# Kernel optimization log

Hardware: AMD Instinct MI355X
Metric: run time of the kernel (lower is better)

## Reference

```python
import jax, jax.numpy as jnp
import numpy as np

HEADS = 16
ROT_DIM = 32  # RotaryEmbedding(dim=32), interleaved (GPT-J style) as in rotary_embedding_torch
THETA = 10000.0


def _rope(x):
    # x: (B, H, S, hd); rotate first ROT_DIM dims, pass through the rest
    S = x.shape[-2]
    inv_freq = 1.0 / (THETA ** (jnp.arange(0, ROT_DIM, 2, dtype=jnp.float32) / ROT_DIM))  # (ROT_DIM/2,)
    ang = jnp.arange(S, dtype=jnp.float32)[:, None] * inv_freq[None, :]                   # (S, ROT_DIM/2)
    ang = jnp.repeat(ang, 2, axis=-1)                                                     # (S, ROT_DIM) interleaved
    cos, sin = jnp.cos(ang), jnp.sin(ang)
    xr, xp = x[..., :ROT_DIM], x[..., ROT_DIM:]
    # rotate_half, interleaved pairs: (x1, x2) -> (-x2, x1)
    x2 = xr.reshape(*xr.shape[:-1], ROT_DIM // 2, 2)
    xr_half = jnp.stack([-x2[..., 1], x2[..., 0]], axis=-1).reshape(xr.shape)
    xr = xr * cos + xr_half * sin
    return jnp.concatenate([xr, xp], axis=-1)


def _split_heads(x, H):
    # (S, B, D) -> (B, H, S, hd)
    S, B, D = x.shape
    return x.transpose(1, 0, 2).reshape(B, S, H, D // H).transpose(0, 2, 1, 3)


def setup_inputs() -> dict:
    key = jax.random.key(0)
    ks = jax.random.split(key, 11)
    S, B, D = 2048, 2, 1024
    f = lambda k, shp, s=1.0: jax.random.normal(k, shp, dtype=jnp.float32) * s
    return {
        "Q": f(ks[0], (S, B, D)),
        "K": f(ks[1], (S, B, D)),
        "V": f(ks[2], (S, B, D)),
        "Wq": f(ks[3], (D, D), 0.02), "bq": f(ks[4], (D,), 0.02),
        "Wk": f(ks[5], (D, D), 0.02), "bk": f(ks[6], (D,), 0.02),
        "Wv": f(ks[7], (D, D), 0.02), "bv": f(ks[8], (D,), 0.02),
        "Wo": f(ks[9], (D, D), 0.02), "bo": f(ks[10], (D,), 0.02),
    }


def reference(Q, K, V, Wq, bq, Wk, bk, Wv, bv, Wo, bo):
    S, B, D = Q.shape
    H = HEADS
    hd = D // H
    q = _rope(_split_heads(Q @ Wq.T + bq, H))   # (B, H, S, hd)
    k = _rope(_split_heads(K @ Wk.T + bk, H))
    v = _split_heads(V @ Wv.T + bv, H)
    scores = jnp.einsum("bhqd,bhkd->bhqk", q, k) / jnp.sqrt(jnp.float32(hd))
    probs = jax.nn.softmax(scores, axis=-1)
    out = jnp.einsum("bhqk,bhkd->bhqd", probs, v)  # (B, H, S, hd)
    out = out.transpose(0, 2, 1, 3).reshape(B, S, D).transpose(1, 0, 2)  # (S, B, D)
    return out @ Wo.T + bo
```

## Files before the change

### kernel.cpp

```cpp
#include <hip/hip_runtime.h>
#include <hip/hip_bf16.h>
#include <hip/hip_fp16.h>

#define S_LEN  2048
#define BATCH  2
#define DMODEL 1024
#define NHEADS 16
#define HD     64
#define MROWS  4096
#define LD     72
#define NT     (S_LEN / 64)

using f16 = _Float16;
typedef __attribute__((ext_vector_type(8))) _Float16 f16x8;
typedef __attribute__((ext_vector_type(4))) _Float16 f16x4;
typedef __attribute__((ext_vector_type(4))) float    f32x4;

__device__ __forceinline__ void gload16(const void* g, void* l)
{
    __builtin_amdgcn_global_load_lds((const __attribute__((address_space(1))) void*)g,
                                     (__attribute__((address_space(3))) void*)l, 16, 0, 0);
}

__global__ __launch_bounds__(256) void rope_table(float* __restrict__ rc, float* __restrict__ rs)
{
    int idx = blockIdx.x * 256 + threadIdx.x;
    int s = idx >> 4, i = idx & 15;
    float inv = powf(10000.0f, -(float)(2 * i) / 32.0f);
    float ang = (float)s * inv;
    rc[idx] = cosf(ang);
    rs[idx] = sinf(ang);
}

__global__ __launch_bounds__(256) void cvt_all(
    const float* __restrict__ Q, const float* __restrict__ K, const float* __restrict__ V,
    const float* __restrict__ Wq, const float* __restrict__ Wk, const float* __restrict__ Wv,
    const float* __restrict__ Wo, f16* __restrict__ dst)
{
    const int z = blockIdx.y;
    const float* src; size_t off; int n8;
    switch (z) {
        case 0:  src = Q;  off = 0;        n8 = 524288; break;
        case 1:  src = K;  off = 4194304;  n8 = 524288; break;
        case 2:  src = V;  off = 8388608;  n8 = 524288; break;
        case 3:  src = Wq; off = 12582912; n8 = 131072; break;
        case 4:  src = Wk; off = 13631488; n8 = 131072; break;
        case 5:  src = Wv; off = 14680064; n8 = 131072; break;
        default: src = Wo; off = 15728640; n8 = 131072; break;
    }
    int i = blockIdx.x * 256 + threadIdx.x;
    if (i >= n8) return;
    const float4* s = reinterpret_cast<const float4*>(src) + (size_t)i * 2;
    float4 v0 = s[0], v1 = s[1];
    f16x8 h = { (f16)v0.x, (f16)v0.y, (f16)v0.z, (f16)v0.w,
                (f16)v1.x, (f16)v1.y, (f16)v1.z, (f16)v1.w };
    reinterpret_cast<f16x8*>(dst + off)[i] = h;
}

__global__ __launch_bounds__(256) void proj_gemm_h(
    const f16* __restrict__ Xq, const f16* __restrict__ Xk, const f16* __restrict__ Xv,
    const f16* __restrict__ Wq, const f16* __restrict__ Wk, const f16* __restrict__ Wv,
    const float* __restrict__ bq, const float* __restrict__ bk, const float* __restrict__ bv,
    f16* __restrict__ qo, f16* __restrict__ ko, f16* __restrict__ vo,
    const float* __restrict__ rc, const float* __restrict__ rs)
{
    const int mode = blockIdx.z;
    const f16* X     = (mode == 0) ? Xq : (mode == 1) ? Xk : Xv;
    const f16* W     = (mode == 0) ? Wq : (mode == 1) ? Wk : Wv;
    const float* bias = (mode == 0) ? bq : (mode == 1) ? bk : bv;

    __shared__ f16 Al[128 * 32];
    __shared__ f16 Bl[128 * 32];

    const int t = threadIdx.x, lane = t & 63, wid = t >> 6;
    const int q15 = lane & 15, g = lane >> 4;
    const int wr = wid >> 1, wc = wid & 1;
    const int m0 = blockIdx.x * 128, n0 = blockIdx.y * 128;

    const int srow = wid * 16 + (lane >> 2);
    const int scol = (lane & 3) * 8;
    const f16* Xg = X + (size_t)(m0 + srow) * DMODEL + scol;
    const f16* Wg = W + (size_t)(n0 + srow) * DMODEL + scol;
    f16* al0 = &Al[(wid * 16) * 32];
    f16* al1 = &Al[(wid * 16 + 64) * 32];
    f16* bl0 = &Bl[(wid * 16) * 32];
    f16* bl1 = &Bl[(wid * 16 + 64) * 32];

    f32x4 acc[4][4];
    #pragma unroll
    for (int m = 0; m < 4; m++)
        #pragma unroll
        for (int n = 0; n < 4; n++)
            acc[m][n] = f32x4{0.f, 0.f, 0.f, 0.f};

    for (int k0 = 0; k0 < DMODEL; k0 += 32) {
        __syncthreads();
        gload16(Xg + k0, al0);
        gload16(Xg + (size_t)64 * DMODEL + k0, al1);
        gload16(Wg + k0, bl0);
        gload16(Wg + (size_t)64 * DMODEL + k0, bl1);
        __syncthreads();

        f16x8 a[4], b[4];
        #pragma unroll
        for (int m = 0; m < 4; m++)
            a[m] = *reinterpret_cast<const f16x8*>(&Al[(wr * 64 + m * 16 + q15) * 32 + g * 8]);
        #pragma unroll
        for (int n = 0; n < 4; n++)
            b[n] = *reinterpret_cast<const f16x8*>(&Bl[(wc * 64 + n * 16 + q15) * 32 + g * 8]);
        #pragma unroll
        for (int m = 0; m < 4; m++)
            #pragma unroll
            for (int n = 0; n < 4; n++)
                acc[m][n] = __builtin_amdgcn_mfma_f32_16x16x32_f16(a[m], b[n], acc[m][n], 0, 0, 0);
    }

    const int rowb = m0 + wr * 64, colb = n0 + wc * 64;
    #pragma unroll
    for (int n = 0; n < 4; n++) {
        int cN = colb + n * 16 + q15;
        float bvv = bias[cN];
        int h = cN >> 6, d = cN & 63;
        #pragma unroll
        for (int m = 0; m < 4; m++) {
            #pragma unroll
            for (int rg = 0; rg < 4; rg++) {
                int r = rowb + m * 16 + g * 4 + rg;
                int s = r >> 1, bi = r & 1;
                float val = acc[m][n][rg] + bvv;
                if (mode < 2) {
                    float pv = __shfl_xor(val, 1);
                    if (d < 32) {
                        int fi = d >> 1;
                        float cc = rc[s * 16 + fi], ss = rs[s * 16 + fi];
                        val = ((d & 1) == 0) ? val * cc - pv * ss : val * cc + pv * ss;
                    }
                    if (mode == 0) val *= 0.18033688f;
                    ((mode == 0) ? qo : ko)[(((size_t)bi * NHEADS + h) * S_LEN + s) * HD + d] = (f16)val;
                } else {
                    vo[(((size_t)bi * NHEADS + h) * HD + d) * S_LEN + s] = (f16)val;
                }
            }
        }
    }
}

__global__ __launch_bounds__(256) void out_gemm_h(
    const f16* __restrict__ X, const f16* __restrict__ W,
    const float* __restrict__ bias, float* __restrict__ out)
{
    __shared__ f16 Al[128 * 32];
    __shared__ f16 Bl[128 * 32];

    const int t = threadIdx.x, lane = t & 63, wid = t >> 6;
    const int q15 = lane & 15, g = lane >> 4;
    const int wr = wid >> 1, wc = wid & 1;
    const int m0 = blockIdx.x * 128, n0 = blockIdx.y * 128;

    const int srow = wid * 16 + (lane >> 2);
    const int scol = (lane & 3) * 8;
    const f16* Xg = X + (size_t)(m0 + srow) * DMODEL + scol;
    const f16* Wg = W + (size_t)(n0 + srow) * DMODEL + scol;
    f16* al0 = &Al[(wid * 16) * 32];
    f16* al1 = &Al[(wid * 16 + 64) * 32];
    f16* bl0 = &Bl[(wid * 16) * 32];
    f16* bl1 = &Bl[(wid * 16 + 64) * 32];

    f32x4 acc[4][4];
    #pragma unroll
    for (int m = 0; m < 4; m++)
        #pragma unroll
        for (int n = 0; n < 4; n++)
            acc[m][n] = f32x4{0.f, 0.f, 0.f, 0.f};

    for (int k0 = 0; k0 < DMODEL; k0 += 32) {
        __syncthreads();
        gload16(Xg + k0, al0);
        gload16(Xg + (size_t)64 * DMODEL + k0, al1);
        gload16(Wg + k0, bl0);
        gload16(Wg + (size_t)64 * DMODEL + k0, bl1);
        __syncthreads();

        f16x8 a[4], b[4];
        #pragma unroll
        for (int m = 0; m < 4; m++)
            a[m] = *reinterpret_cast<const f16x8*>(&Al[(wr * 64 + m * 16 + q15) * 32 + g * 8]);
        #pragma unroll
        for (int n = 0; n < 4; n++)
            b[n] = *reinterpret_cast<const f16x8*>(&Bl[(wc * 64 + n * 16 + q15) * 32 + g * 8]);
        #pragma unroll
        for (int m = 0; m < 4; m++)
            #pragma unroll
            for (int n = 0; n < 4; n++)
                acc[m][n] = __builtin_amdgcn_mfma_f32_16x16x32_f16(a[m], b[n], acc[m][n], 0, 0, 0);
    }

    const int rowb = m0 + wr * 64, colb = n0 + wc * 64;
    #pragma unroll
    for (int n = 0; n < 4; n++) {
        int cN = colb + n * 16 + q15;
        float bvv = bias[cN];
        #pragma unroll
        for (int m = 0; m < 4; m++) {
            #pragma unroll
            for (int rg = 0; rg < 4; rg++) {
                int r = rowb + m * 16 + g * 4 + rg;
                out[(size_t)r * DMODEL + cN] = acc[m][n][rg] + bvv;
            }
        }
    }
}

__global__ __launch_bounds__(256) void proj_gemm(
    const float* __restrict__ Xq, const float* __restrict__ Xk, const float* __restrict__ Xv,
    const float* __restrict__ Wq, const float* __restrict__ Wk, const float* __restrict__ Wv,
    const float* __restrict__ bq, const float* __restrict__ bk, const float* __restrict__ bv,
    f16* __restrict__ qo, f16* __restrict__ ko, f16* __restrict__ vo,
    const float* __restrict__ rc, const float* __restrict__ rs)
{
    const int mode = blockIdx.z;
    const float* X    = (mode == 0) ? Xq : (mode == 1) ? Xk : Xv;
    const float* W    = (mode == 0) ? Wq : (mode == 1) ? Wk : Wv;
    const float* bias = (mode == 0) ? bq : (mode == 1) ? bk : bv;

    __shared__ f16 Al[128 * 40];
    __shared__ f16 Bl[128 * 40];

    const int t = threadIdx.x;
    const int lane = t & 63, wid = t >> 6;
    const int wr = wid >> 1, wc = wid & 1;
    const int m0 = blockIdx.x * 128, n0 = blockIdx.y * 128;

    f32x4 acc[4][4];
    #pragma unroll
    for (int m = 0; m < 4; m++)
        #pragma unroll
        for (int n = 0; n < 4; n++)
            acc[m][n] = f32x4{0.f, 0.f, 0.f, 0.f};

    for (int k0 = 0; k0 < DMODEL; k0 += 32) {
        __syncthreads();
        #pragma unroll
        for (int i = 0; i < 2; i++) {
            int e = (i * 256 + t) * 8;
            int r = e >> 5, c = e & 31;
            {
                const float* src = &X[(size_t)(m0 + r) * DMODEL + k0 + c];
                float4 v0 = *reinterpret_cast<const float4*>(src);
                float4 v1 = *reinterpret_cast<const float4*>(src + 4);
                f16x8 h = { (f16)v0.x, (f16)v0.y, (f16)v0.z, (f16)v0.w,
                            (f16)v1.x, (f16)v1.y, (f16)v1.z, (f16)v1.w };
                *reinterpret_cast<f16x8*>(&Al[r * 40 + c]) = h;
            }
            {
                const float* src = &W[(size_t)(n0 + r) * DMODEL + k0 + c];
                float4 v0 = *reinterpret_cast<const float4*>(src);
                float4 v1 = *reinterpret_cast<const float4*>(src + 4);
                f16x8 h = { (f16)v0.x, (f16)v0.y, (f16)v0.z, (f16)v0.w,
                            (f16)v1.x, (f16)v1.y, (f16)v1.z, (f16)v1.w };
                *reinterpret_cast<f16x8*>(&Bl[r * 40 + c]) = h;
            }
        }
        __syncthreads();
        f16x8 a[4], b[4];
        #pragma unroll
        for (int m = 0; m < 4; m++)
            a[m] = *reinterpret_cast<const f16x8*>(&Al[(wr * 64 + m * 16 + (lane & 15)) * 40 + (lane >> 4) * 8]);
        #pragma unroll
        for (int n = 0; n < 4; n++)
            b[n] = *reinterpret_cast<const f16x8*>(&Bl[(wc * 64 + n * 16 + (lane & 15)) * 40 + (lane >> 4) * 8]);
        #pragma unroll
        for (int m = 0; m < 4; m++)
            #pragma unroll
            for (int n = 0; n < 4; n++)
                acc[m][n] = __builtin_amdgcn_mfma_f32_16x16x32_f16(a[m], b[n], acc[m][n], 0, 0, 0);
    }

    const int rowb = m0 + wr * 64, colb = n0 + wc * 64;
    #pragma unroll
    for (int n = 0; n < 4; n++) {
        int cN = colb + n * 16 + (lane & 15);
        float bvv = bias[cN];
        int h = cN >> 6, d = cN & 63;
        #pragma unroll
        for (int m = 0; m < 4; m++) {
            #pragma unroll
            for (int rg = 0; rg < 4; rg++) {
                int r = rowb + m * 16 + (lane >> 4) * 4 + rg;
                int s = r >> 1, bi = r & 1;
                float val = acc[m][n][rg] + bvv;
                if (mode < 2) {
                    float pv = __shfl_xor(val, 1);
                    if (d < 32) {
                        int fi = d >> 1;
                        float cc = rc[s * 16 + fi], ss = rs[s * 16 + fi];
                        val = ((d & 1) == 0) ? val * cc - pv * ss : val * cc + pv * ss;
                    }
                    if (mode == 0) val *= 0.18033688f;
                    ((mode == 0) ? qo : ko)[(((size_t)bi * NHEADS + h) * S_LEN + s) * HD + d] = (f16)val;
                } else {
                    vo[(((size_t)bi * NHEADS + h) * HD + d) * S_LEN + s] = (f16)val;
                }
            }
        }
    }
}

__global__ __launch_bounds__(256) void out_gemm(
    const f16* __restrict__ X, const float* __restrict__ W,
    const float* __restrict__ bias, float* __restrict__ out)
{
    __shared__ f16 Al[128 * 40];
    __shared__ f16 Bl[128 * 40];

    const int t = threadIdx.x;
    const int lane = t & 63, wid = t >> 6;
    const int wr = wid >> 1, wc = wid & 1;
    const int m0 = blockIdx.x * 128, n0 = blockIdx.y * 128;

    f32x4 acc[4][4];
    #pragma unroll
    for (int m = 0; m < 4; m++)
        #pragma unroll
        for (int n = 0; n < 4; n++)
            acc[m][n] = f32x4{0.f, 0.f, 0.f, 0.f};

    for (int k0 = 0; k0 < DMODEL; k0 += 32) {
        __syncthreads();
        #pragma unroll
        for (int i = 0; i < 2; i++) {
            int e = (i * 256 + t) * 8;
            int r = e >> 5, c = e & 31;
            *reinterpret_cast<uint4*>(&Al[r * 40 + c]) =
                *reinterpret_cast<const uint4*>(&X[(size_t)(m0 + r) * DMODEL + k0 + c]);
            {
                const float* src = &W[(size_t)(n0 + r) * DMODEL + k0 + c];
                float4 v0 = *reinterpret_cast<const float4*>(src);
                float4 v1 = *reinterpret_cast<const float4*>(src + 4);
                f16x8 h = { (f16)v0.x, (f16)v0.y, (f16)v0.z, (f16)v0.w,
                            (f16)v1.x, (f16)v1.y, (f16)v1.z, (f16)v1.w };
                *reinterpret_cast<f16x8*>(&Bl[r * 40 + c]) = h;
            }
        }
        __syncthreads();
        f16x8 a[4], b[4];
        #pragma unroll
        for (int m = 0; m < 4; m++)
            a[m] = *reinterpret_cast<const f16x8*>(&Al[(wr * 64 + m * 16 + (lane & 15)) * 40 + (lane >> 4) * 8]);
        #pragma unroll
        for (int n = 0; n < 4; n++)
            b[n] = *reinterpret_cast<const f16x8*>(&Bl[(wc * 64 + n * 16 + (lane & 15)) * 40 + (lane >> 4) * 8]);
        #pragma unroll
        for (int m = 0; m < 4; m++)
            #pragma unroll
            for (int n = 0; n < 4; n++)
                acc[m][n] = __builtin_amdgcn_mfma_f32_16x16x32_f16(a[m], b[n], acc[m][n], 0, 0, 0);
    }

    const int rowb = m0 + wr * 64, colb = n0 + wc * 64;
    #pragma unroll
    for (int n = 0; n < 4; n++) {
        int cN = colb + n * 16 + (lane & 15);
        float bvv = bias[cN];
        #pragma unroll
        for (int m = 0; m < 4; m++) {
            #pragma unroll
            for (int rg = 0; rg < 4; rg++) {
                int r = rowb + m * 16 + (lane >> 4) * 4 + rg;
                out[(size_t)r * DMODEL + cN] = acc[m][n][rg] + bvv;
            }
        }
    }
}

__global__ __launch_bounds__(512) void attn_fwd(
    const f16* __restrict__ qb, const f16* __restrict__ kb,
    const f16* __restrict__ vt, f16* __restrict__ ctx)
{
    __shared__ f16 Kl[2][64 * 64];
    __shared__ f16 Vl[3][64 * 64];
    __shared__ f16 Pl[2][8 * 16 * LD];

    const int t = threadIdx.x, lane = t & 63, wid = t >> 6;
    const int q15 = lane & 15, g = lane >> 4;
    const int sw = q15 & 7;
    const int bh = blockIdx.y;
    const int q0 = blockIdx.x * 128 + wid * 16;

    const f16* qptr = qb + ((size_t)bh * S_LEN + q0) * HD;
    f16x8 qf0 = *reinterpret_cast<const f16x8*>(&qptr[q15 * HD + g * 8]);
    f16x8 qf1 = *reinterpret_cast<const f16x8*>(&qptr[q15 * HD + g * 8 + 32]);

    f32x4 ctxa[4];
    #pragma unroll
    for (int i = 0; i < 4; i++) ctxa[i] = f32x4{0.f, 0.f, 0.f, 0.f};
    float mrun = -3.0e38f, lrun = 0.f;

    const int srow = t >> 3;
    const int sslot = (t & 7) ^ (srow & 7);
    const f16* kg = kb + (size_t)bh * S_LEN * HD + (size_t)srow * HD + sslot * 8;
    const f16* vg = vt + (size_t)bh * HD * S_LEN + (size_t)srow * S_LEN + sslot * 8;
    const int lds_wbase = wid * 512;
    const int poff = wid * (16 * LD);

    gload16(kg, &Kl[0][lds_wbase]);
    gload16(vg, &Vl[0][lds_wbase]);
    __syncthreads();

    int kbuf = 0;
    int vprev = 2, vcur = 0, vnext = 1;

    for (int kt = 0; kt < NT; kt++) {
        if (kt + 1 < NT) {
            gload16(kg + (size_t)(kt + 1) * 64 * HD, &Kl[kbuf ^ 1][lds_wbase]);
            gload16(vg + (size_t)(kt + 1) * 64,      &Vl[vnext][lds_wbase]);
        }
        const f16* Kc = Kl[kbuf];

        f32x4 sc[4];
        __builtin_amdgcn_s_setprio(1);
        #pragma unroll
        for (int f = 0; f < 4; f++) {
            f16x8 kf0 = *reinterpret_cast<const f16x8*>(&Kc[(f * 16 + q15) * 64 + ((g ^ sw) * 8)]);
            f16x8 kf1 = *reinterpret_cast<const f16x8*>(&Kc[(f * 16 + q15) * 64 + (((g + 4) ^ sw) * 8)]);
            f32x4 z = {0.f, 0.f, 0.f, 0.f};
            z = __builtin_amdgcn_mfma_f32_16x16x32_f16(kf0, qf0, z, 0, 0, 0);
            sc[f] = __builtin_amdgcn_mfma_f32_16x16x32_f16(kf1, qf1, z, 0, 0, 0);
        }
        if (kt > 0) {
            const f16* Vp = Vl[vprev];
            const f16* pr = &Pl[(kt & 1) ^ 1][poff];
            #pragma unroll
            for (int c = 0; c < 2; c++) {
                f16x8 pfr = *reinterpret_cast<const f16x8*>(&pr[q15 * LD + g * 8 + c * 32]);
                #pragma unroll
                for (int n = 0; n < 4; n++) {
                    f16x8 vf = *reinterpret_cast<const f16x8*>(&Vp[(n * 16 + q15) * 64 + (((g + c * 4) ^ sw) * 8)]);
                    ctxa[n] = __builtin_amdgcn_mfma_f32_16x16x32_f16(vf, pfr, ctxa[n], 0, 0, 0);
                }
            }
        }
        __builtin_amdgcn_s_setprio(0);

        float pmf[4];
        #pragma unroll
        for (int f = 0; f < 4; f++)
            pmf[f] = fmaxf(fmaxf(sc[f][0], sc[f][1]), fmaxf(sc[f][2], sc[f][3]));
        float pm = fmaxf(fmaxf(pmf[0], pmf[1]), fmaxf(pmf[2], pmf[3]));
        if (!__all(pm - mrun <= 8.0f)) {
            float pmax = fmaxf(pm, __shfl_xor(pm, 16));
            pmax = fmaxf(pmax, __shfl_xor(pmax, 32));
            float mnew = fmaxf(mrun, pmax);
            float scale = __builtin_amdgcn_exp2f(mrun - mnew);
            lrun *= scale;
            #pragma unroll
            for (int n = 0; n < 4; n++) {
                ctxa[n][0] *= scale; ctxa[n][1] *= scale;
                ctxa[n][2] *= scale; ctxa[n][3] *= scale;
            }
            mrun = mnew;
        }
        float tsum = 0.f;
        #pragma unroll
        for (int f = 0; f < 4; f++)
            #pragma unroll
            for (int rg = 0; rg < 4; rg++) {
                float p = __builtin_amdgcn_exp2f(sc[f][rg] - mrun);
                sc[f][rg] = p;
                tsum += p;
            }
        lrun += tsum;

        f16* pw = &Pl[kt & 1][poff];
        #pragma unroll
        for (int f = 0; f < 4; f++) {
            f16x4 pwv = { (f16)sc[f][0], (f16)sc[f][1], (f16)sc[f][2], (f16)sc[f][3] };
            *reinterpret_cast<f16x4*>(&pw[q15 * LD + f * 16 + g * 4]) = pwv;
        }

        __syncthreads();
        kbuf ^= 1;
        int tmp = vprev; vprev = vcur; vcur = vnext; vnext = tmp;
    }

    {
        const f16* Vp = Vl[vprev];
        const f16* pr = &Pl[(NT - 1) & 1][poff];
        #pragma unroll
        for (int c = 0; c < 2; c++) {
            f16x8 pfr = *reinterpret_cast<const f16x8*>(&pr[q15 * LD + g * 8 + c * 32]);
            #pragma unroll
            for (int n = 0; n < 4; n++) {
                f16x8 vf = *reinterpret_cast<const f16x8*>(&Vp[(n * 16 + q15) * 64 + (((g + c * 4) ^ sw) * 8)]);
                ctxa[n] = __builtin_amdgcn_mfma_f32_16x16x32_f16(vf, pfr, ctxa[n], 0, 0, 0);
            }
        }
    }

    lrun += __shfl_xor(lrun, 16);
    lrun += __shfl_xor(lrun, 32);
    const int bi = bh >> 4, h = bh & 15;
    const int s = q0 + q15;
    float inv = 1.0f / lrun;
    f16* outp = &ctx[((size_t)s * BATCH + bi) * DMODEL + h * HD];
    #pragma unroll
    for (int n = 0; n < 4; n++) {
        f16x4 o = { (f16)(ctxa[n][0] * inv), (f16)(ctxa[n][1] * inv),
                    (f16)(ctxa[n][2] * inv), (f16)(ctxa[n][3] * inv) };
        *reinterpret_cast<f16x4*>(&outp[n * 16 + g * 4]) = o;
    }
}

extern "C" void kernel_launch(void* const* d_in, const int* in_sizes, int n_in,
                              void* d_out, int out_size, void* d_ws, size_t ws_size,
                              hipStream_t stream)
{
    const float* Q  = (const float*)d_in[0];
    const float* K  = (const float*)d_in[1];
    const float* V  = (const float*)d_in[2];
    const float* Wq = (const float*)d_in[3];
    const float* bq = (const float*)d_in[4];
    const float* Wk = (const float*)d_in[5];
    const float* bk = (const float*)d_in[6];
    const float* Wv = (const float*)d_in[7];
    const float* bv = (const float*)d_in[8];
    const float* Wo = (const float*)d_in[9];
    const float* bo = (const float*)d_in[10];
    float* out = (float*)d_out;

    char* w = (char*)d_ws;
    const size_t MBc = 1024 * 1024;
    const size_t NEED_FAST = 56 * MBc + 256 * 1024;

    if (ws_size >= NEED_FAST) {
        f16* cvtb = (f16*)w;
        f16* Xqh = cvtb;
        f16* Xkh = cvtb + 4194304;
        f16* Xvh = cvtb + 8388608;
        f16* Wqh = cvtb + 12582912;
        f16* Wkh = cvtb + 13631488;
        f16* Wvh = cvtb + 14680064;
        f16* Woh = cvtb + 15728640;
        float* rc = (float*)(w + 32 * MBc);
        float* rs = rc + 32768;
        f16* qbuf = (f16*)(w + 32 * MBc + 256 * 1024);
        f16* kbuf = qbuf + 4194304;
        f16* vtb  = kbuf + 4194304;
        f16* ctxb = Xqh;

        rope_table<<<(S_LEN * 16) / 256, 256, 0, stream>>>(rc, rs);
        cvt_all<<<dim3(2048, 7), 256, 0, stream>>>(Q, K, V, Wq, Wk, Wv, Wo, cvtb);
        proj_gemm_h<<<dim3(MROWS / 128, DMODEL / 128, 3), 256, 0, stream>>>(
            Xqh, Xkh, Xvh, Wqh, Wkh, Wvh, bq, bk, bv, qbuf, kbuf, vtb, rc, rs);
        attn_fwd<<<dim3(S_LEN / 128, BATCH * NHEADS), 512, 0, stream>>>(qbuf, kbuf, vtb, ctxb);
        out_gemm_h<<<dim3(MROWS / 128, DMODEL / 128), 256, 0, stream>>>(ctxb, Woh, bo, out);
    } else {
        const size_t szT = (size_t)S_LEN * 16 * sizeof(float);
        const size_t szQ = (size_t)MROWS * DMODEL * sizeof(f16);
        float* rc  = (float*)(w);
        float* rs  = (float*)(w + szT);
        f16* qbuf = (f16*)(w + 2 * szT);
        f16* kbuf = (f16*)(w + 2 * szT + szQ);
        f16* vtb  = (f16*)(w + 2 * szT + 2 * szQ);
        f16* ctxb = (f16*)(w + 2 * szT + 3 * szQ);

        rope_table<<<(S_LEN * 16) / 256, 256, 0, stream>>>(rc, rs);
        proj_gemm<<<dim3(MROWS / 128, DMODEL / 128, 3), 256, 0, stream>>>(
            Q, K, V, Wq, Wk, Wv, bq, bk, bv, qbuf, kbuf, vtb, rc, rs);
        attn_fwd<<<dim3(S_LEN / 128, BATCH * NHEADS), 512, 0, stream>>>(qbuf, kbuf, vtb, ctxb);
        out_gemm<<<dim3(MROWS / 128, DMODEL / 128), 256, 0, stream>>>(ctxb, Wo, bo, out);
    }
}
```

Before: 150.5 us.

## Fuse fp32-to-fp16 activation conversion into projection GEMM loads

The separate conversion pass over Q/K/V is removed. Only the weights are converted now, and the projection GEMM streams fp32 activations straight into LDS through a XOR-swizzled layout, converting to fp16 when fragments are read. This avoids writing and re-reading 24 MB of fp16 activation copies. In exchange each GEMM tile loads twice as many bytes of A from global memory and LDS, and LDS use per block grows.

```diff
diff --git a/kernel.cpp b/kernel.cpp
--- a/kernel.cpp
+++ b/kernel.cpp
@@ -32,24 +32,14 @@
     rs[idx] = sinf(ang);
 }
 
-__global__ __launch_bounds__(256) void cvt_all(
-    const float* __restrict__ Q, const float* __restrict__ K, const float* __restrict__ V,
-    const float* __restrict__ Wq, const float* __restrict__ Wk, const float* __restrict__ Wv,
-    const float* __restrict__ Wo, f16* __restrict__ dst)
+__global__ __launch_bounds__(256) void cvt_w(
+    const float* __restrict__ Wq, const float* __restrict__ Wk,
+    const float* __restrict__ Wv, const float* __restrict__ Wo, f16* __restrict__ dst)
 {
     const int z = blockIdx.y;
-    const float* src; size_t off; int n8;
-    switch (z) {
-        case 0:  src = Q;  off = 0;        n8 = 524288; break;
-        case 1:  src = K;  off = 4194304;  n8 = 524288; break;
-        case 2:  src = V;  off = 8388608;  n8 = 524288; break;
-        case 3:  src = Wq; off = 12582912; n8 = 131072; break;
-        case 4:  src = Wk; off = 13631488; n8 = 131072; break;
-        case 5:  src = Wv; off = 14680064; n8 = 131072; break;
-        default: src = Wo; off = 15728640; n8 = 131072; break;
-    }
+    const float* src = (z == 0) ? Wq : (z == 1) ? Wk : (z == 2) ? Wv : Wo;
+    const size_t off = (size_t)z * 1048576;
     int i = blockIdx.x * 256 + threadIdx.x;
-    if (i >= n8) return;
     const float4* s = reinterpret_cast<const float4*>(src) + (size_t)i * 2;
     float4 v0 = s[0], v1 = s[1];
     f16x8 h = { (f16)v0.x, (f16)v0.y, (f16)v0.z, (f16)v0.w,
@@ -58,31 +48,36 @@
 }
 
 __global__ __launch_bounds__(256) void proj_gemm_h(
-    const f16* __restrict__ Xq, const f16* __restrict__ Xk, const f16* __restrict__ Xv,
+    const float* __restrict__ Xq, const float* __restrict__ Xk, const float* __restrict__ Xv,
     const f16* __restrict__ Wq, const f16* __restrict__ Wk, const f16* __restrict__ Wv,
     const float* __restrict__ bq, const float* __restrict__ bk, const float* __restrict__ bv,
     f16* __restrict__ qo, f16* __restrict__ ko, f16* __restrict__ vo,
     const float* __restrict__ rc, const float* __restrict__ rs)
 {
     const int mode = blockIdx.z;
-    const f16* X     = (mode == 0) ? Xq : (mode == 1) ? Xk : Xv;
+    const float* X   = (mode == 0) ? Xq : (mode == 1) ? Xk : Xv;
     const f16* W     = (mode == 0) ? Wq : (mode == 1) ? Wk : Wv;
     const float* bias = (mode == 0) ? bq : (mode == 1) ? bk : bv;
 
-    __shared__ f16 Al[128 * 32];
-    __shared__ f16 Bl[128 * 32];
+    __shared__ __align__(16) float Afp[128 * 32];
+    __shared__ __align__(16) f16   Bl[128 * 32];
 
     const int t = threadIdx.x, lane = t & 63, wid = t >> 6;
     const int q15 = lane & 15, g = lane >> 4;
     const int wr = wid >> 1, wc = wid & 1;
     const int m0 = blockIdx.x * 128, n0 = blockIdx.y * 128;
 
-    const int srow = wid * 16 + (lane >> 2);
-    const int scol = (lane & 3) * 8;
-    const f16* Xg = X + (size_t)(m0 + srow) * DMODEL + scol;
-    const f16* Wg = W + (size_t)(n0 + srow) * DMODEL + scol;
-    f16* al0 = &Al[(wid * 16) * 32];
-    f16* al1 = &Al[(wid * 16 + 64) * 32];
+    const int srowA = wid * 32 + (lane >> 3);
+    const int sslotA = (lane & 7) ^ (lane >> 3);
+    const float* XgA = X + (size_t)(m0 + srowA) * DMODEL + sslotA * 4;
+    float* aB0 = &Afp[(wid * 32 + 0) * 32];
+    float* aB1 = &Afp[(wid * 32 + 8) * 32];
+    float* aB2 = &Afp[(wid * 32 + 16) * 32];
+    float* aB3 = &Afp[(wid * 32 + 24) * 32];
+
+    const int srowB = wid * 16 + (lane >> 2);
+    const int scolB = (lane & 3) * 8;
+    const f16* Wg = W + (size_t)(n0 + srowB) * DMODEL + scolB;
     f16* bl0 = &Bl[(wid * 16) * 32];
     f16* bl1 = &Bl[(wid * 16 + 64) * 32];
 
@@ -95,16 +90,24 @@
 
     for (int k0 = 0; k0 < DMODEL; k0 += 32) {
         __syncthreads();
-        gload16(Xg + k0, al0);
-        gload16(Xg + (size_t)64 * DMODEL + k0, al1);
+        gload16(XgA + k0, aB0);
+        gload16(XgA + (size_t)8 * DMODEL + k0, aB1);
+        gload16(XgA + (size_t)16 * DMODEL + k0, aB2);
+        gload16(XgA + (size_t)24 * DMODEL + k0, aB3);
         gload16(Wg + k0, bl0);
         gload16(Wg + (size_t)64 * DMODEL + k0, bl1);
         __syncthreads();
 
         f16x8 a[4], b[4];
-        #pragma unroll
-        for (int m = 0; m < 4; m++)
-            a[m] = *reinterpret_cast<const f16x8*>(&Al[(wr * 64 + m * 16 + q15) * 32 + g * 8]);
+        const int p = q15 & 7;
+        #pragma unroll
+        for (int m = 0; m < 4; m++) {
+            const float* ap = &Afp[(wr * 64 + m * 16 + q15) * 32];
+            float4 v0 = *reinterpret_cast<const float4*>(&ap[((2 * g) ^ p) * 4]);
+            float4 v1 = *reinterpret_cast<const float4*>(&ap[((2 * g + 1) ^ p) * 4]);
+            a[m] = f16x8{ (f16)v0.x, (f16)v0.y, (f16)v0.z, (f16)v0.w,
+                          (f16)v1.x, (f16)v1.y, (f16)v1.z, (f16)v1.w };
+        }
         #pragma unroll
         for (int n = 0; n < 4; n++)
             b[n] = *reinterpret_cast<const f16x8*>(&Bl[(wc * 64 + n * 16 + q15) * 32 + g * 8]);
@@ -149,8 +152,8 @@
     const f16* __restrict__ X, const f16* __restrict__ W,
     const float* __restrict__ bias, float* __restrict__ out)
 {
-    __shared__ f16 Al[128 * 32];
-    __shared__ f16 Bl[128 * 32];
+    __shared__ __align__(16) f16 Al[128 * 32];
+    __shared__ __align__(16) f16 Bl[128 * 32];
 
     const int t = threadIdx.x, lane = t & 63, wid = t >> 6;
     const int q15 = lane & 15, g = lane >> 4;
@@ -530,28 +533,24 @@
 
     char* w = (char*)d_ws;
     const size_t MBc = 1024 * 1024;
-    const size_t NEED_FAST = 56 * MBc + 256 * 1024;
+    const size_t NEED_FAST = 40 * MBc + 256 * 1024;
 
     if (ws_size >= NEED_FAST) {
-        f16* cvtb = (f16*)w;
-        f16* Xqh = cvtb;
-        f16* Xkh = cvtb + 4194304;
-        f16* Xvh = cvtb + 8388608;
-        f16* Wqh = cvtb + 12582912;
-        f16* Wkh = cvtb + 13631488;
-        f16* Wvh = cvtb + 14680064;
-        f16* Woh = cvtb + 15728640;
-        float* rc = (float*)(w + 32 * MBc);
+        f16* Wqh = (f16*)w;
+        f16* Wkh = Wqh + 1048576;
+        f16* Wvh = Wqh + 2097152;
+        f16* Woh = Wqh + 3145728;
+        float* rc = (float*)(w + 8 * MBc);
         float* rs = rc + 32768;
-        f16* qbuf = (f16*)(w + 32 * MBc + 256 * 1024);
+        f16* qbuf = (f16*)(w + 8 * MBc + 256 * 1024);
         f16* kbuf = qbuf + 4194304;
         f16* vtb  = kbuf + 4194304;
-        f16* ctxb = Xqh;
+        f16* ctxb = vtb + 4194304;
 
         rope_table<<<(S_LEN * 16) / 256, 256, 0, stream>>>(rc, rs);
-        cvt_all<<<dim3(2048, 7), 256, 0, stream>>>(Q, K, V, Wq, Wk, Wv, Wo, cvtb);
+        cvt_w<<<dim3(512, 4), 256, 0, stream>>>(Wq, Wk, Wv, Wo, Wqh);
         proj_gemm_h<<<dim3(MROWS / 128, DMODEL / 128, 3), 256, 0, stream>>>(
-            Xqh, Xkh, Xvh, Wqh, Wkh, Wvh, bq, bk, bv, qbuf, kbuf, vtb, rc, rs);
+            Q, K, V, Wqh, Wkh, Wvh, bq, bk, bv, qbuf, kbuf, vtb, rc, rs);
         attn_fwd<<<dim3(S_LEN / 128, BATCH * NHEADS), 512, 0, stream>>>(qbuf, kbuf, vtb, ctxb);
         out_gemm_h<<<dim3(MROWS / 128, DMODEL / 128), 256, 0, stream>>>(ctxb, Woh, bo, out);
     } else {
```

Measured after the change: 146.2 us (median of 5 runs). 1.03x faster.
